# Kernel tuning notes

Hardware: AMD Instinct MI355X
Metric: run time of the kernel (lower is better)

The kernel has to match this reference:

```python
import jax, jax.numpy as jnp
import numpy as np

BN_EPS = 1e-5
# regular 3x3 kernel grid offsets: row0 = dy, row1 = dx, kernel positions in row-major order
REG = jnp.array([[-1, -1, -1, 0, 0, 0, 1, 1, 1],
                 [-1,  0,  1, -1, 0, 1, -1, 0, 1]], dtype=jnp.float32)


def conv3x3(x, w, b):
    y = jax.lax.conv_general_dilated(x, w, window_strides=(1, 1),
                                     padding=((1, 1), (1, 1)),
                                     dimension_numbers=('NCHW', 'OIHW', 'NCHW'))
    return y + b[None, :, None, None]


def deform_conv3x3(x, dy, dx, w):
    # x: [N,C,H,W]; dy,dx: [N,9,H,W] per-kernel-tap offsets; w: [O,C,3,3]
    N, C, H, W = x.shape
    K = 9
    ky = jnp.repeat(jnp.arange(3), 3)   # [0,0,0,1,1,1,2,2,2]
    kx = jnp.tile(jnp.arange(3), 3)     # [0,1,2,0,1,2,0,1,2]
    # sampling positions: p = p_out - pad + k*dilation + offset (stride=1, pad=dil=1)
    py = dy + (jnp.arange(H) - 1)[None, None, :, None] + ky[None, :, None, None].astype(x.dtype)
    px = dx + (jnp.arange(W) - 1)[None, None, None, :] + kx[None, :, None, None].astype(x.dtype)
    y0 = jnp.floor(py)
    x0 = jnp.floor(px)
    wy = py - y0  # bilinear weights
    wx = px - x0
    y0i = y0.astype(jnp.int32)
    x0i = x0.astype(jnp.int32)
    nidx = jnp.arange(N)[:, None, None, None]

    def gather(yi, xi):
        valid = ((yi >= 0) & (yi < H) & (xi >= 0) & (xi < W)).astype(x.dtype)
        v = x[nidx, :, jnp.clip(yi, 0, H - 1), jnp.clip(xi, 0, W - 1)]  # [N,K,H,W,C]
        return v * valid[..., None]

    sampled = (gather(y0i,     x0i)     * ((1 - wy) * (1 - wx))[..., None]
             + gather(y0i,     x0i + 1) * ((1 - wy) * wx)[..., None]
             + gather(y0i + 1, x0i)     * (wy * (1 - wx))[..., None]
             + gather(y0i + 1, x0i + 1) * (wy * wx)[..., None])  # [N,K,H,W,C]
    O = w.shape[0]
    return jnp.einsum('nkhwc,ock->nohw', sampled, w.reshape(O, C, K))


def setup_inputs() -> dict:
    key = jax.random.key(0)
    ks = jax.random.split(key, 12)
    N, C, H, W = 2, 256, 96, 96
    O = 256
    sc = 1.0 / np.sqrt(C * 9)
    return {
        'x': jax.random.normal(ks[0], (N, C, H, W), jnp.float32),
        'mask_attention': jax.random.normal(ks[1], (N, C, H, W), jnp.float32),
        'w_tm': jax.random.normal(ks[2], (4, C, 3, 3), jnp.float32) * sc,
        'b_tm': jax.random.normal(ks[3], (4,), jnp.float32) * 0.01,
        'w_tr': jax.random.normal(ks[4], (2, C, 3, 3), jnp.float32) * sc,
        'b_tr': jax.random.normal(ks[5], (2,), jnp.float32) * 0.01,
        'w_deform': jax.random.normal(ks[6], (O, C, 3, 3), jnp.float32) * sc,
        'bn_gamma': jnp.ones((O,), jnp.float32),
        'bn_beta': jnp.zeros((O,), jnp.float32),
        'bn_mean': jax.random.normal(ks[7], (O,), jnp.float32) * 0.01,
        'bn_var': jax.random.uniform(ks[8], (O,), jnp.float32, 0.5, 1.5),
    }


def reference(x, mask_attention, w_tm, b_tm, w_tr, b_tr, w_deform,
              bn_gamma, bn_beta, bn_mean, bn_var):
    # mask_attention is overwritten by x in the original forward; ignored.
    N, C, H, W = x.shape
    tm = conv3x3(x, w_tm, b_tm)                       # [N,4,H,W]
    T = tm.transpose(0, 2, 3, 1).reshape(N, H, W, 2, 2)
    off = jnp.einsum('nhwij,jk->nhwik', T, REG) - REG  # [N,H,W,2,9], (T-I)@REG
    tr = conv3x3(x, w_tr, b_tr)                        # [N,2,H,W]
    off = off + tr.transpose(0, 2, 3, 1)[..., None]    # broadcast translation to all 9 taps
    dy = off[..., 0, :].transpose(0, 3, 1, 2)          # [N,9,H,W]
    dx = off[..., 1, :].transpose(0, 3, 1, 2)
    out = deform_conv3x3(x, dy, dx, w_deform)          # [N,O,H,W]
    inv = jax.lax.rsqrt(bn_var + BN_EPS)
    out = (out - bn_mean[None, :, None, None]) * (inv * bn_gamma)[None, :, None, None] \
          + bn_beta[None, :, None, None]
    return jax.nn.relu(out + x)
```

## Files before the change

### kernel.cpp

```cpp
#include <hip/hip_runtime.h>
#include <stdint.h>

#define H_ 96
#define W_ 96
#define C_ 256
#define O_ 256
#define N_ 2
#define HW_ (H_*W_)
#define M_ (N_*HW_)
#define GK 2304

typedef __bf16 bf16x8 __attribute__((ext_vector_type(8)));
typedef float f32x4 __attribute__((ext_vector_type(4)));
typedef unsigned short us4 __attribute__((ext_vector_type(4)));
typedef unsigned short us8 __attribute__((ext_vector_type(8)));

__device__ __forceinline__ unsigned short f2bf(float f) {
  union { float f; unsigned int u; } v; v.f = f;
  unsigned int u = v.u;
  return (unsigned short)((u + 0x7fffu + ((u >> 16) & 1u)) >> 16);
}
__device__ __forceinline__ float bf2f(unsigned short h) {
  union { unsigned int u; float f; } v; v.u = ((unsigned int)h) << 16;
  return v.f;
}

__global__ __launch_bounds__(256) void k_pre(const float* __restrict__ x,
                                             const float* __restrict__ w_df,
                                             const float* __restrict__ w_tm,
                                             const float* __restrict__ w_tr,
                                             unsigned short* __restrict__ xt,
                                             unsigned short* __restrict__ wfrag,
                                             unsigned short* __restrict__ w6p) {
  const int b = blockIdx.x;
  const int tid = threadIdx.x;
  if (b < 288) {
    __shared__ unsigned short tile[128][130];
    const int pt = b % 72;
    const int ch = (b / 72) & 1;
    const int n  = b / 144;
    const int p0 = pt * 128, c0 = ch * 128;
    const float* xp = x + (size_t)n * C_ * HW_;
    unsigned short* xtp = xt + (size_t)n * C_ * HW_;
    const int tx = tid & 31, ty = tid >> 5;
#pragma unroll
    for (int pass = 0; pass < 16; pass++) {
      const int c = pass * 8 + ty;
      const f32x4 v = *(const f32x4*)(xp + (size_t)(c0 + c) * HW_ + p0 + tx * 4);
#pragma unroll
      for (int i = 0; i < 4; i++) tile[tx * 4 + i][c] = f2bf(v[i]);
    }
    __syncthreads();
    const int wave = tid >> 6, lane = tid & 63;
    const int l32 = lane & 31, ph = lane >> 5;
#pragma unroll
    for (int pass = 0; pass < 16; pass++) {
      const int p = pass * 8 + wave * 2 + ph;
      us4 v;
#pragma unroll
      for (int i = 0; i < 4; i++) v[i] = tile[p][l32 * 4 + i];
      *(us4*)(xtp + (size_t)(p0 + p) * C_ + c0 + l32 * 4) = v;
    }
  } else if (b < 576) {
    const int base = (b - 288) * 2048 + tid * 8;
    const int l  = (base >> 3) & 63;
    const int g  = (base >> 9) & 15;
    const int ks = (base >> 13) & 7;
    const int t  = base >> 16;
    const int o  = g * 16 + (l & 15);
    const int c  = ks * 32 + (l >> 4) * 8;
    us8 res;
#pragma unroll
    for (int j = 0; j < 8; j++) res[j] = f2bf(w_df[(size_t)(o * 256 + c + j) * 9 + t]);
    *(us8*)(wfrag + base) = res;
  } else {
    int idx = (b - 576) * 256 + tid;
    int t = idx >> 12;
    int r = idx & 4095;
    int j = r >> 8;
    int c = r & 255;
    float v = 0.f;
    if (j < 4) v = w_tm[(size_t)(j * C_ + c) * 9 + t];
    else if (j < 6) v = w_tr[(size_t)((j - 4) * C_ + c) * 9 + t];
    w6p[idx] = f2bf(v);
  }
}

__global__ __launch_bounds__(256, 4) void k_fused(const unsigned short* __restrict__ xt,
                                                  const unsigned short* __restrict__ Wfrag,
                                                  const unsigned short* __restrict__ w6p,
                                                  const float* __restrict__ b_tm,
                                                  const float* __restrict__ b_tr,
                                                  const float* __restrict__ xres,
                                                  const float* __restrict__ gamma,
                                                  const float* __restrict__ beta,
                                                  const float* __restrict__ mean,
                                                  const float* __restrict__ var,
                                                  float* __restrict__ out) {
  __shared__ unsigned short As[2][16 * 256] __attribute__((aligned(16)));
  __shared__ float sred[4][16][8];
  __shared__ float coords_s[16][9][2];
  const int tid = threadIdx.x;
  const int wave = tid >> 6, lane = tid & 63;
  const int row = lane & 15, quad = lane >> 4;
  const int bm = (blockIdx.x & 7) * 144 + (blockIdx.x >> 3);
  const int m0 = bm * 16;
  const int n = m0 / HW_;
  const int sr = tid >> 4;
  const int cg = tid & 15;

  {
    const int hw0 = m0 - n * HW_;
    const int h = hw0 / W_;
    const int w0 = hw0 - h * W_;
    const int cq = wave * 64;
    f32x4 oacc = {0.f, 0.f, 0.f, 0.f};
    const bf16x8 zero8 = {};
#pragma unroll
    for (int t = 0; t < 9; t++) {
      const int ty = t / 3, tx = t % 3;
      const int y = h + ty - 1;
      if (y < 0 || y >= H_) continue;
      const int xx = w0 + row + tx - 1;
      const bool valid = (xx >= 0) && (xx < W_);
      const int xc = min(max(xx, 0), W_ - 1);
      const unsigned short* arow =
          xt + (size_t)((n * H_ + y) * W_ + xc) * C_ + cq + quad * 8;
      const unsigned short* brow =
          w6p + (size_t)(t * 16 + row) * C_ + cq + quad * 8;
#pragma unroll
      for (int ks = 0; ks < 2; ks++) {
        bf16x8 av = *(const bf16x8*)(const void*)(arow + ks * 32);
        if (!valid) av = zero8;
        bf16x8 bv = *(const bf16x8*)(const void*)(brow + ks * 32);
        oacc = __builtin_amdgcn_mfma_f32_16x16x32_bf16(av, bv, oacc, 0, 0, 0);
      }
    }
    if (row < 6) {
#pragma unroll
      for (int r = 0; r < 4; r++) sred[wave][quad * 4 + r][row] = oacc[r];
    }
  }
  __syncthreads();
  if (wave == 0 && lane < 16) {
    const int hwm = m0 + lane - n * HW_;
    const int h = hwm / W_, w = hwm - h * W_;
    float a[6];
#pragma unroll
    for (int j = 0; j < 6; j++)
      a[j] = sred[0][lane][j] + sred[1][lane][j] + sred[2][lane][j] + sred[3][lane][j];
    const float tm0 = a[0] + b_tm[0];
    const float tm1 = a[1] + b_tm[1];
    const float tm2 = a[2] + b_tm[2];
    const float tm3 = a[3] + b_tm[3];
    const float tr0 = a[4] + b_tr[0];
    const float tr1 = a[5] + b_tr[1];
#pragma unroll
    for (int t = 0; t < 9; t++) {
      const float ry = (float)(t / 3) - 1.f;
      const float rx = (float)(t % 3) - 1.f;
      coords_s[lane][t][0] = (float)h + tr0 + tm0 * ry + tm1 * rx;
      coords_s[lane][t][1] = (float)w + tr1 + tm2 * ry + tm3 * rx;
    }
  }
  __syncthreads();

  f32x4 acc[4] = {};
  float cw0, cw1, cw2, cw3;
  int cb0, cb1, cb2, cb3;
  us8 u0[4], u1[4];

#define PREP(TAP)                                                              \
  {                                                                            \
    const float py = coords_s[sr][TAP][0];                                     \
    const float px = coords_s[sr][TAP][1];                                     \
    const float fy = floorf(py), fx = floorf(px);                              \
    const float wy = py - fy, wx = px - fx;                                    \
    const int y0 = (int)fy, x0 = (int)fx;                                      \
    const int y1 = y0 + 1, x1 = x0 + 1;                                        \
    const float vy0 = (y0 >= 0 && y0 < H_) ? 1.f : 0.f;                        \
    const float vy1 = (y1 >= 0 && y1 < H_) ? 1.f : 0.f;                        \
    const float vx0 = (x0 >= 0 && x0 < W_) ? 1.f : 0.f;                        \
    const float vx1 = (x1 >= 0 && x1 < W_) ? 1.f : 0.f;                        \
    cw0 = (1.f - wy) * (1.f - wx) * vy0 * vx0;                                 \
    cw1 = (1.f - wy) * wx * vy0 * vx1;                                         \
    cw2 = wy * (1.f - wx) * vy1 * vx0;                                         \
    cw3 = wy * wx * vy1 * vx1;                                                 \
    const int cy0 = min(max(y0, 0), H_ - 1), cy1 = min(max(y1, 0), H_ - 1);    \
    const int cx0 = min(max(x0, 0), W_ - 1), cx1 = min(max(x1, 0), W_ - 1);    \
    cb0 = ((n * H_ + cy0) * W_ + cx0) * C_;                                    \
    cb1 = ((n * H_ + cy0) * W_ + cx1) * C_;                                    \
    cb2 = ((n * H_ + cy1) * W_ + cx0) * C_;                                    \
    cb3 = ((n * H_ + cy1) * W_ + cx1) * C_;                                    \
  }

#define LOAD_CORNERS()                                                         \
  {                                                                            \
    const int cc = cg * 16;                                                    \
    u0[0] = *(const us8*)(xt + cb0 + cc); u1[0] = *(const us8*)(xt + cb0 + cc + 8); \
    u0[1] = *(const us8*)(xt + cb1 + cc); u1[1] = *(const us8*)(xt + cb1 + cc + 8); \
    u0[2] = *(const us8*)(xt + cb2 + cc); u1[2] = *(const us8*)(xt + cb2 + cc + 8); \
    u0[3] = *(const us8*)(xt + cb3 + cc); u1[3] = *(const us8*)(xt + cb3 + cc + 8); \
  }

  PREP(0);
  LOAD_CORNERS();
  for (int tap = 0; tap < 9; tap++) {
    unsigned short* __restrict__ asb = As[tap & 1];
    {
      us8 r0, r1;
#pragma unroll
      for (int e = 0; e < 8; e++) {
        r0[e] = f2bf(cw0 * bf2f(u0[0][e]) + cw1 * bf2f(u0[1][e]) +
                     cw2 * bf2f(u0[2][e]) + cw3 * bf2f(u0[3][e]));
        r1[e] = f2bf(cw0 * bf2f(u1[0][e]) + cw1 * bf2f(u1[1][e]) +
                     cw2 * bf2f(u1[2][e]) + cw3 * bf2f(u1[3][e]));
      }
      const int q0 = cg * 2, q1 = cg * 2 + 1;
      const int s0 = (q0 & 24) | ((q0 ^ sr) & 7);
      const int s1 = (q1 & 24) | ((q1 ^ sr) & 7);
      *(us8*)(void*)&asb[sr * 256 + s0 * 8] = r0;
      *(us8*)(void*)&asb[sr * 256 + s1 * 8] = r1;
    }
    __syncthreads();

    const unsigned short* wfTap = Wfrag + (size_t)(tap * 8) * 8192 + (wave * 4) * 512 + lane * 8;
    bf16x8 bv[4];
#pragma unroll
    for (int ot = 0; ot < 4; ot++) bv[ot] = *(const bf16x8*)(const void*)(wfTap + ot * 512);

    if (tap < 8) {
      PREP(tap + 1);
      LOAD_CORNERS();
    }

#pragma unroll
    for (int ks = 0; ks < 8; ks++) {
      const int q = ks * 4 + quad;
      const int slot = (q & 24) | ((q ^ row) & 7);
      const bf16x8 av = *(const bf16x8*)(const void*)&asb[row * 256 + slot * 8];
      bf16x8 bn[4];
      if (ks < 7) {
        const unsigned short* wfn = wfTap + (size_t)(ks + 1) * 8192;
#pragma unroll
        for (int ot = 0; ot < 4; ot++) bn[ot] = *(const bf16x8*)(const void*)(wfn + ot * 512);
      }
#pragma unroll
      for (int ot = 0; ot < 4; ot++)
        acc[ot] = __builtin_amdgcn_mfma_f32_16x16x32_bf16(av, bv[ot], acc[ot], 0, 0, 0);
      if (ks < 7) {
#pragma unroll
        for (int ot = 0; ot < 4; ot++) bv[ot] = bn[ot];
      }
    }
    __syncthreads();
  }

  const int hwb = m0 - n * HW_ + quad * 4;
#pragma unroll
  for (int ot = 0; ot < 4; ot++) {
    const int o = wave * 64 + ot * 16 + row;
    const float sc = rsqrtf(var[o] + 1e-5f) * gamma[o];
    const float bi = beta[o] - mean[o] * sc;
    const size_t obase = (size_t)(n * O_ + o) * HW_ + hwb;
    const f32x4 rv = *(const f32x4*)(xres + obase);
    f32x4 ov;
#pragma unroll
    for (int r = 0; r < 4; r++) ov[r] = fmaxf(acc[ot][r] * sc + bi + rv[r], 0.f);
    *(f32x4*)(out + obase) = ov;
  }
}

extern "C" void kernel_launch(void* const* d_in, const int* in_sizes, int n_in,
                              void* d_out, int out_size, void* d_ws, size_t ws_size,
                              hipStream_t stream) {
  const float* x     = (const float*)d_in[0];
  const float* w_tm  = (const float*)d_in[2];
  const float* b_tm  = (const float*)d_in[3];
  const float* w_tr  = (const float*)d_in[4];
  const float* b_tr  = (const float*)d_in[5];
  const float* w_df  = (const float*)d_in[6];
  const float* gamma = (const float*)d_in[7];
  const float* beta  = (const float*)d_in[8];
  const float* mean  = (const float*)d_in[9];
  const float* var   = (const float*)d_in[10];
  float* out = (float*)d_out;

  char* ws = (char*)d_ws;
  unsigned short* xt    = (unsigned short*)(ws);
  unsigned short* wfrag = (unsigned short*)(ws + 9437184);
  unsigned short* w6p   = (unsigned short*)(ws + 9437184 + 1179648);

  k_pre<<<720, 256, 0, stream>>>(x, w_df, w_tm, w_tr, xt, wfrag, w6p);
  k_fused<<<1152, 256, 0, stream>>>(xt, wfrag, w6p, b_tm, b_tr, x,
                                    gamma, beta, mean, var, out);
}
```

Measured before the change: 186.0 us.

## Double M-tile to 32 rows per block to reuse weight fragments

```diff
diff --git a/kernel.cpp b/kernel.cpp
--- a/kernel.cpp
+++ b/kernel.cpp
@@ -86,7 +86,7 @@
   }
 }
 
-__global__ __launch_bounds__(256, 4) void k_fused(const unsigned short* __restrict__ xt,
+__global__ __launch_bounds__(256, 3) void k_fused(const unsigned short* __restrict__ xt,
                                                   const unsigned short* __restrict__ Wfrag,
                                                   const unsigned short* __restrict__ w6p,
                                                   const float* __restrict__ b_tm,
@@ -97,14 +97,14 @@
                                                   const float* __restrict__ mean,
                                                   const float* __restrict__ var,
                                                   float* __restrict__ out) {
-  __shared__ unsigned short As[2][16 * 256] __attribute__((aligned(16)));
+  __shared__ unsigned short As[2][32 * 256] __attribute__((aligned(16)));
   __shared__ float sred[4][16][8];
-  __shared__ float coords_s[16][9][2];
+  __shared__ float coords_s[32][9][2];
   const int tid = threadIdx.x;
   const int wave = tid >> 6, lane = tid & 63;
   const int row = lane & 15, quad = lane >> 4;
-  const int bm = (blockIdx.x & 7) * 144 + (blockIdx.x >> 3);
-  const int m0 = bm * 16;
+  const int bm = (blockIdx.x & 7) * 72 + (blockIdx.x >> 3);
+  const int m0 = bm * 32;
   const int n = m0 / HW_;
   const int sr = tid >> 4;
   const int cg = tid & 15;
@@ -113,7 +113,8 @@
     const int hw0 = m0 - n * HW_;
     const int h = hw0 / W_;
     const int w0 = hw0 - h * W_;
-    const int cq = wave * 64;
+    const int rh = wave >> 1;
+    const int cq = (wave & 1) * 128;
     f32x4 oacc = {0.f, 0.f, 0.f, 0.f};
     const bf16x8 zero8 = {};
 #pragma unroll
@@ -121,7 +122,7 @@
       const int ty = t / 3, tx = t % 3;
       const int y = h + ty - 1;
       if (y < 0 || y >= H_) continue;
-      const int xx = w0 + row + tx - 1;
+      const int xx = w0 + rh * 16 + row + tx - 1;
       const bool valid = (xx >= 0) && (xx < W_);
       const int xc = min(max(xx, 0), W_ - 1);
       const unsigned short* arow =
@@ -129,7 +130,7 @@
       const unsigned short* brow =
           w6p + (size_t)(t * 16 + row) * C_ + cq + quad * 8;
 #pragma unroll
-      for (int ks = 0; ks < 2; ks++) {
+      for (int ks = 0; ks < 4; ks++) {
         bf16x8 av = *(const bf16x8*)(const void*)(arow + ks * 32);
         if (!valid) av = zero8;
         bf16x8 bv = *(const bf16x8*)(const void*)(brow + ks * 32);
@@ -142,13 +143,14 @@
     }
   }
   __syncthreads();
-  if (wave == 0 && lane < 16) {
-    const int hwm = m0 + lane - n * HW_;
+  if (wave < 2 && lane < 16) {
+    const int rg = wave * 16 + lane;
+    const int hwm = m0 + rg - n * HW_;
     const int h = hwm / W_, w = hwm - h * W_;
     float a[6];
 #pragma unroll
     for (int j = 0; j < 6; j++)
-      a[j] = sred[0][lane][j] + sred[1][lane][j] + sred[2][lane][j] + sred[3][lane][j];
+      a[j] = sred[wave * 2][lane][j] + sred[wave * 2 + 1][lane][j];
     const float tm0 = a[0] + b_tm[0];
     const float tm1 = a[1] + b_tm[1];
     const float tm2 = a[2] + b_tm[2];
@@ -159,21 +161,21 @@
     for (int t = 0; t < 9; t++) {
       const float ry = (float)(t / 3) - 1.f;
       const float rx = (float)(t % 3) - 1.f;
-      coords_s[lane][t][0] = (float)h + tr0 + tm0 * ry + tm1 * rx;
-      coords_s[lane][t][1] = (float)w + tr1 + tm2 * ry + tm3 * rx;
+      coords_s[rg][t][0] = (float)h + tr0 + tm0 * ry + tm1 * rx;
+      coords_s[rg][t][1] = (float)w + tr1 + tm2 * ry + tm3 * rx;
     }
   }
   __syncthreads();
 
-  f32x4 acc[4] = {};
-  float cw0, cw1, cw2, cw3;
-  int cb0, cb1, cb2, cb3;
-  us8 u0[4], u1[4];
-
-#define PREP(TAP)                                                              \
+  f32x4 acc0[4] = {}, acc1[4] = {};
+  float cwA[4], cwB[4];
+  int cbA[4], cbB[4];
+  us8 uA0[4], uA1[4], uB0[4], uB1[4];
+
+#define PREP1(TAP, R, CW, CB)                                                  \
   {                                                                            \
-    const float py = coords_s[sr][TAP][0];                                     \
-    const float px = coords_s[sr][TAP][1];                                     \
+    const float py = coords_s[R][TAP][0];                                      \
+    const float px = coords_s[R][TAP][1];                                      \
     const float fy = floorf(py), fx = floorf(px);                              \
     const float wy = py - fy, wx = px - fx;                                    \
     const int y0 = (int)fy, x0 = (int)fx;                                      \
@@ -182,63 +184,78 @@
     const float vy1 = (y1 >= 0 && y1 < H_) ? 1.f : 0.f;                        \
     const float vx0 = (x0 >= 0 && x0 < W_) ? 1.f : 0.f;                        \
     const float vx1 = (x1 >= 0 && x1 < W_) ? 1.f : 0.f;                        \
-    cw0 = (1.f - wy) * (1.f - wx) * vy0 * vx0;                                 \
-    cw1 = (1.f - wy) * wx * vy0 * vx1;                                         \
-    cw2 = wy * (1.f - wx) * vy1 * vx0;                                         \
-    cw3 = wy * wx * vy1 * vx1;                                                 \
+    CW[0] = (1.f - wy) * (1.f - wx) * vy0 * vx0;                               \
+    CW[1] = (1.f - wy) * wx * vy0 * vx1;                                       \
+    CW[2] = wy * (1.f - wx) * vy1 * vx0;                                       \
+    CW[3] = wy * wx * vy1 * vx1;                                               \
     const int cy0 = min(max(y0, 0), H_ - 1), cy1 = min(max(y1, 0), H_ - 1);    \
     const int cx0 = min(max(x0, 0), W_ - 1), cx1 = min(max(x1, 0), W_ - 1);    \
-    cb0 = ((n * H_ + cy0) * W_ + cx0) * C_;                                    \
-    cb1 = ((n * H_ + cy0) * W_ + cx1) * C_;                                    \
-    cb2 = ((n * H_ + cy1) * W_ + cx0) * C_;                                    \
-    cb3 = ((n * H_ + cy1) * W_ + cx1) * C_;                                    \
-  }
-
-#define LOAD_CORNERS()                                                         \
+    CB[0] = ((n * H_ + cy0) * W_ + cx0) * C_;                                  \
+    CB[1] = ((n * H_ + cy0) * W_ + cx1) * C_;                                  \
+    CB[2] = ((n * H_ + cy1) * W_ + cx0) * C_;                                  \
+    CB[3] = ((n * H_ + cy1) * W_ + cx1) * C_;                                  \
+  }
+
+#define LOADC1(CB, U0, U1)                                                     \
   {                                                                            \
     const int cc = cg * 16;                                                    \
-    u0[0] = *(const us8*)(xt + cb0 + cc); u1[0] = *(const us8*)(xt + cb0 + cc + 8); \
-    u0[1] = *(const us8*)(xt + cb1 + cc); u1[1] = *(const us8*)(xt + cb1 + cc + 8); \
-    u0[2] = *(const us8*)(xt + cb2 + cc); u1[2] = *(const us8*)(xt + cb2 + cc + 8); \
-    u0[3] = *(const us8*)(xt + cb3 + cc); u1[3] = *(const us8*)(xt + cb3 + cc + 8); \
-  }
-
-  PREP(0);
-  LOAD_CORNERS();
+    U0[0] = *(const us8*)(xt + CB[0] + cc); U1[0] = *(const us8*)(xt + CB[0] + cc + 8); \
+    U0[1] = *(const us8*)(xt + CB[1] + cc); U1[1] = *(const us8*)(xt + CB[1] + cc + 8); \
+    U0[2] = *(const us8*)(xt + CB[2] + cc); U1[2] = *(const us8*)(xt + CB[2] + cc + 8); \
+    U0[3] = *(const us8*)(xt + CB[3] + cc); U1[3] = *(const us8*)(xt + CB[3] + cc + 8); \
+  }
+
+#define LERP8(DST, U, CW)                                                      \
+  {                                                                            \
+    _Pragma("unroll")                                                          \
+    for (int e = 0; e < 8; e++)                                                \
+      DST[e] = f2bf(CW[0] * bf2f(U[0][e]) + CW[1] * bf2f(U[1][e]) +            \
+                    CW[2] * bf2f(U[2][e]) + CW[3] * bf2f(U[3][e]));            \
+  }
+
+  PREP1(0, sr, cwA, cbA);
+  PREP1(0, sr + 16, cwB, cbB);
+  LOADC1(cbA, uA0, uA1);
+  LOADC1(cbB, uB0, uB1);
+
   for (int tap = 0; tap < 9; tap++) {
     unsigned short* __restrict__ asb = As[tap & 1];
     {
-      us8 r0, r1;
-#pragma unroll
-      for (int e = 0; e < 8; e++) {
-        r0[e] = f2bf(cw0 * bf2f(u0[0][e]) + cw1 * bf2f(u0[1][e]) +
-                     cw2 * bf2f(u0[2][e]) + cw3 * bf2f(u0[3][e]));
-        r1[e] = f2bf(cw0 * bf2f(u1[0][e]) + cw1 * bf2f(u1[1][e]) +
-                     cw2 * bf2f(u1[2][e]) + cw3 * bf2f(u1[3][e]));
-      }
       const int q0 = cg * 2, q1 = cg * 2 + 1;
       const int s0 = (q0 & 24) | ((q0 ^ sr) & 7);
       const int s1 = (q1 & 24) | ((q1 ^ sr) & 7);
+      us8 r0, r1;
+      LERP8(r0, uA0, cwA);
+      LERP8(r1, uA1, cwA);
       *(us8*)(void*)&asb[sr * 256 + s0 * 8] = r0;
       *(us8*)(void*)&asb[sr * 256 + s1 * 8] = r1;
-    }
+      LERP8(r0, uB0, cwB);
+      LERP8(r1, uB1, cwB);
+      *(us8*)(void*)&asb[(sr + 16) * 256 + s0 * 8] = r0;
+      *(us8*)(void*)&asb[(sr + 16) * 256 + s1 * 8] = r1;
+    }
+
+    const unsigned short* wfTap =
+        Wfrag + (size_t)(tap * 8) * 8192 + wave * 2048 + lane * 8;
+    bf16x8 bv[4];
+#pragma unroll
+    for (int ot = 0; ot < 4; ot++) bv[ot] = *(const bf16x8*)(const void*)(wfTap + ot * 512);
+
     __syncthreads();
 
-    const unsigned short* wfTap = Wfrag + (size_t)(tap * 8) * 8192 + (wave * 4) * 512 + lane * 8;
-    bf16x8 bv[4];
-#pragma unroll
-    for (int ot = 0; ot < 4; ot++) bv[ot] = *(const bf16x8*)(const void*)(wfTap + ot * 512);
-
     if (tap < 8) {
-      PREP(tap + 1);
-      LOAD_CORNERS();
+      PREP1(tap + 1, sr, cwA, cbA);
+      PREP1(tap + 1, sr + 16, cwB, cbB);
+      LOADC1(cbA, uA0, uA1);
+      LOADC1(cbB, uB0, uB1);
     }
 
 #pragma unroll
     for (int ks = 0; ks < 8; ks++) {
       const int q = ks * 4 + quad;
       const int slot = (q & 24) | ((q ^ row) & 7);
-      const bf16x8 av = *(const bf16x8*)(const void*)&asb[row * 256 + slot * 8];
+      const bf16x8 av0 = *(const bf16x8*)(const void*)&asb[row * 256 + slot * 8];
+      const bf16x8 av1 = *(const bf16x8*)(const void*)&asb[(row + 16) * 256 + slot * 8];
       bf16x8 bn[4];
       if (ks < 7) {
         const unsigned short* wfn = wfTap + (size_t)(ks + 1) * 8192;
@@ -247,13 +264,15 @@
       }
 #pragma unroll
       for (int ot = 0; ot < 4; ot++)
-        acc[ot] = __builtin_amdgcn_mfma_f32_16x16x32_bf16(av, bv[ot], acc[ot], 0, 0, 0);
+        acc0[ot] = __builtin_amdgcn_mfma_f32_16x16x32_bf16(av0, bv[ot], acc0[ot], 0, 0, 0);
+#pragma unroll
+      for (int ot = 0; ot < 4; ot++)
+        acc1[ot] = __builtin_amdgcn_mfma_f32_16x16x32_bf16(av1, bv[ot], acc1[ot], 0, 0, 0);
       if (ks < 7) {
 #pragma unroll
         for (int ot = 0; ot < 4; ot++) bv[ot] = bn[ot];
       }
     }
-    __syncthreads();
   }
 
   const int hwb = m0 - n * HW_ + quad * 4;
@@ -262,12 +281,17 @@
     const int o = wave * 64 + ot * 16 + row;
     const float sc = rsqrtf(var[o] + 1e-5f) * gamma[o];
     const float bi = beta[o] - mean[o] * sc;
-    const size_t obase = (size_t)(n * O_ + o) * HW_ + hwb;
-    const f32x4 rv = *(const f32x4*)(xres + obase);
+    const size_t ob0 = (size_t)(n * O_ + o) * HW_ + hwb;
+    f32x4 rv = *(const f32x4*)(xres + ob0);
     f32x4 ov;
 #pragma unroll
-    for (int r = 0; r < 4; r++) ov[r] = fmaxf(acc[ot][r] * sc + bi + rv[r], 0.f);
-    *(f32x4*)(out + obase) = ov;
+    for (int r = 0; r < 4; r++) ov[r] = fmaxf(acc0[ot][r] * sc + bi + rv[r], 0.f);
+    *(f32x4*)(out + ob0) = ov;
+    const size_t ob1 = ob0 + 16;
+    rv = *(const f32x4*)(xres + ob1);
+#pragma unroll
+    for (int r = 0; r < 4; r++) ov[r] = fmaxf(acc1[ot][r] * sc + bi + rv[r], 0.f);
+    *(f32x4*)(out + ob1) = ov;
   }
 }
 
@@ -292,6 +316,6 @@
   unsigned short* w6p   = (unsigned short*)(ws + 9437184 + 1179648);
 
   k_pre<<<720, 256, 0, stream>>>(x, w_df, w_tm, w_tr, xt, wfrag, w6p);
-  k_fused<<<1152, 256, 0, stream>>>(xt, wfrag, w6p, b_tm, b_tr, x,
-                                    gamma, beta, mean, var, out);
-}
+  k_fused<<<576, 256, 0, stream>>>(xt, wfrag, w6p, b_tm, b_tr, x,
+                                   gamma, beta, mean, var, out);
+}
```

After: 177.7 us. 1.05x faster.
